# Optimization experiments

Measured on AMD Instinct MI355X. Metric: run time of the kernel, lower is better.

## Reference

```python
import jax, jax.numpy as jnp
import numpy as np

NU = 0.01 / np.pi  # Burgers viscosity
LAYERS = [2, 128, 128, 128, 128, 1]
N_EQ, N_INIT, N_BND = 131072, 4096, 4096


def setup_inputs() -> dict:
    key = jax.random.key(0)
    ks = jax.random.split(key, 16)
    inp = {
        'tx_equation': jax.random.uniform(ks[0], (N_EQ, 2), dtype=jnp.float32),
        'tx_init': jax.random.uniform(ks[1], (N_INIT, 2), dtype=jnp.float32),
        'tx_bound': jax.random.uniform(ks[2], (N_BND, 2), dtype=jnp.float32),
    }
    # Glorot-normal initialized Dense weights, zero biases (keras defaults in build_network)
    for i, (fin, fout) in enumerate(zip(LAYERS[:-1], LAYERS[1:])):
        std = np.sqrt(2.0 / (fin + fout)).astype(np.float32)
        inp[f'W{i}'] = jax.random.normal(ks[3 + i], (fin, fout), dtype=jnp.float32) * std
        inp[f'b{i}'] = jnp.zeros((fout,), dtype=jnp.float32)
    return inp


def _mlp_scalar(tx, Ws, bs):
    # tx: (2,) -> scalar u. tanh hidden layers, linear output.
    h = tx
    for W, b in zip(Ws[:-1], bs[:-1]):
        h = jnp.tanh(h @ W + b)
    return (h @ Ws[-1] + bs[-1])[0]


def reference(tx_equation, tx_init, tx_bound, W0, b0, W1, b1, W2, b2, W3, b3, W4, b4):
    Ws = [W0, W1, W2, W3, W4]
    bs = [b0, b1, b2, b3, b4]

    def u_s(tx):
        return _mlp_scalar(tx, Ws, bs)

    def u_x_s(tx):
        return jax.grad(u_s)(tx)[1]

    # PDE residual on collocation points
    u = jax.vmap(u_s)(tx_equation)                     # (N,)
    g = jax.vmap(jax.grad(u_s))(tx_equation)           # (N, 2) -> columns (u_t, u_x)
    u_t, u_x = g[:, 0], g[:, 1]
    u_xx = jax.vmap(jax.grad(u_x_s))(tx_equation)[:, 1]  # (N,)
    burgers_eq = (u_t + u * u_x - NU * u_xx)[:, None]     # (N, 1)

    # Initial / boundary predictions (single fused batch like tf.concat in call)
    tx_ib = jnp.concatenate([tx_init, tx_bound], axis=0)
    u_ib = jax.vmap(u_s)(tx_ib)[:, None]
    n_i = tx_init.shape[0]
    return burgers_eq, u_ib[:n_i], u_ib[n_i:]
```

## Files before the change

kernel.cpp:

```cpp
#include <hip/hip_runtime.h>
#include <math.h>

#define NU_F 0.0031830988618379067f
#define HS 136

typedef __attribute__((ext_vector_type(8))) _Float16 half8;
typedef __attribute__((ext_vector_type(4))) _Float16 half4;
typedef __attribute__((ext_vector_type(16))) float f32x16;

__device__ __forceinline__ float fast_tanh(float x) {
    const float e = __builtin_amdgcn_exp2f(x * 2.8853900817779268f);
    const float r = __builtin_amdgcn_rcpf(e + 1.f);
    return fmaf(-2.f, r, 1.f);
}

__global__ void prep_kernel(const float* __restrict__ W1,
                            const float* __restrict__ W2,
                            const float* __restrict__ W3,
                            _Float16* __restrict__ ws)
{
    const int g = blockIdx.x * 256 + threadIdx.x;
    const int l = g >> 14;
    const int r = g & 16383;
    const int n = r & 127;
    const int k = r >> 7;
    const float* W = (l == 0) ? W1 : (l == 1) ? W2 : W3;
    const float w = W[k * 128 + n];
    ws[l * 16384 + (k >> 4) * 2048 + n * 16 + (k & 15)] = (_Float16)w;
}

__launch_bounds__(256, 5)
__global__ void pinn_kernel(const float* __restrict__ tx_eq,
                            const float* __restrict__ tx_init,
                            const float* __restrict__ tx_bnd,
                            const float* __restrict__ W0, const float* __restrict__ b0,
                            const float* __restrict__ b1, const float* __restrict__ b2,
                            const float* __restrict__ b3,
                            const float* __restrict__ W4, const float* __restrict__ b4,
                            const _Float16* __restrict__ wt,
                            float* __restrict__ out)
{
    __shared__ _Float16 Hh[64][HS];

    const int tid   = threadIdx.x;
    const int blk   = blockIdx.x;
    const bool is_eq = (blk < 8192);
    const int w     = tid >> 6;
    const int lane  = tid & 63;
    const int col   = lane & 31;
    const int khalf = lane >> 5;
    const int ncol  = 32 * w + col;
    const int wofs  = ncol * 16 + khalf * 8;

    if (is_eq) {
        const int p  = tid >> 4;
        const int fb = (tid & 15) * 8;
        const float tv = tx_eq[blk * 32 + 2 * p];
        const float xv = tx_eq[blk * 32 + 2 * p + 1];
        const int m0 = 4 * p;
        float vch[4][8];
        #pragma unroll
        for (int j = 0; j < 8; ++j) {
            const int f = fb + j;
            const float w0v = W0[f];
            const float w1v = W0[128 + f];
            const float z = fmaf(tv, w0v, fmaf(xv, w1v, b0[f]));
            const float a = fast_tanh(z);
            const float s = 1.f - a * a;
            vch[0][j] = a;
            vch[1][j] = s * w0v;
            vch[2][j] = s * w1v;
            vch[3][j] = -2.f * a * s * w1v * w1v;
        }
        #pragma unroll
        for (int c = 0; c < 4; ++c) {
            half8 hh;
            #pragma unroll
            for (int j = 0; j < 8; ++j) hh[j] = (_Float16)vch[c][j];
            *(half8*)&Hh[m0 + c][fb] = hh;
        }
    } else {
        const int p  = tid >> 2;
        const int f0 = (tid & 3) * 32;
        const int gp = (blk - 8192) * 64 + p;
        const float* src = (gp < 4096) ? tx_init : tx_bnd;
        const int idx = (gp < 4096) ? gp : gp - 4096;
        const float tv = src[2 * idx];
        const float xv = src[2 * idx + 1];
        #pragma unroll
        for (int g = 0; g < 4; ++g) {
            half8 hh;
            #pragma unroll
            for (int j = 0; j < 8; ++j) {
                const int f = f0 + 8 * g + j;
                hh[j] = (_Float16)fast_tanh(fmaf(tv, W0[f], fmaf(xv, W0[128 + f], b0[f])));
            }
            *(half8*)&Hh[p][f0 + 8 * g] = hh;
        }
    }
    __syncthreads();

    const float* barr[3] = {b1, b2, b3};

    #pragma unroll 1
    for (int layer = 0; layer < 3; ++layer) {
        const _Float16* __restrict__ ph = wt + layer * 16384 + wofs;
        const float bias = barr[layer][ncol];

        half8 q0 = *(const half8*)(ph);
        half8 q1 = *(const half8*)(ph + 2048);
        half8 q2 = *(const half8*)(ph + 4096);
        half8 q3 = *(const half8*)(ph + 6144);
        half8 q4 = *(const half8*)(ph + 8192);
        half8 q5 = *(const half8*)(ph + 10240);
        half8 q6 = *(const half8*)(ph + 12288);
        half8 q7 = *(const half8*)(ph + 14336);

        f32x16 acc0, acc1;
        #pragma unroll
        for (int e = 0; e < 16; ++e) {
            const float v = (is_eq && (e & 3) != 0) ? 0.f : bias;
            acc0[e] = v; acc1[e] = v;
        }

#define KSTEP(KT, Q)                                                          \
        {                                                                     \
            const int k0 = KT * 16 + khalf * 8;                               \
            const half8 ah0 = *(const half8*)&Hh[col][k0];                    \
            const half8 ah1 = *(const half8*)&Hh[32 + col][k0];               \
            acc0 = __builtin_amdgcn_mfma_f32_32x32x16_f16(ah0, Q, acc0, 0, 0, 0); \
            acc1 = __builtin_amdgcn_mfma_f32_32x32x16_f16(ah1, Q, acc1, 0, 0, 0); \
        }
        KSTEP(0, q0) KSTEP(1, q1) KSTEP(2, q2) KSTEP(3, q3)
        KSTEP(4, q4) KSTEP(5, q5) KSTEP(6, q6) KSTEP(7, q7)
#undef KSTEP

        half4 h16[2][4];
        #pragma unroll
        for (int mt = 0; mt < 2; ++mt)
            #pragma unroll
            for (int g = 0; g < 4; ++g) {
                const float A0 = (mt == 0 ? acc0 : acc1)[4 * g + 0];
                const float A1 = (mt == 0 ? acc0 : acc1)[4 * g + 1];
                const float A2 = (mt == 0 ? acc0 : acc1)[4 * g + 2];
                const float A3 = (mt == 0 ? acc0 : acc1)[4 * g + 3];
                half4 hv;
                if (is_eq) {
                    const float t = fast_tanh(A0);
                    const float s = 1.f - t * t;
                    hv[0] = (_Float16)t;
                    hv[1] = (_Float16)(s * A1);
                    hv[2] = (_Float16)(s * A2);
                    hv[3] = (_Float16)fmaf(s, A3, -2.f * t * s * A2 * A2);
                } else {
                    hv[0] = (_Float16)fast_tanh(A0);
                    hv[1] = (_Float16)fast_tanh(A1);
                    hv[2] = (_Float16)fast_tanh(A2);
                    hv[3] = (_Float16)fast_tanh(A3);
                }
                h16[mt][g] = hv;
            }

        __syncthreads();

        #pragma unroll
        for (int mt = 0; mt < 2; ++mt)
            #pragma unroll
            for (int g = 0; g < 4; ++g) {
                const int mrow0 = mt * 32 + 8 * g + 4 * khalf;
                Hh[mrow0 + 0][ncol] = h16[mt][g][0];
                Hh[mrow0 + 1][ncol] = h16[mt][g][1];
                Hh[mrow0 + 2][ncol] = h16[mt][g][2];
                Hh[mrow0 + 3][ncol] = h16[mt][g][3];
            }
        __syncthreads();
    }

    {
        const float b4v = b4[0];
        const int m = tid >> 2;
        const int q = tid & 3;
        float dot = 0.f;
        #pragma unroll
        for (int g = 0; g < 4; ++g) {
            const int f = 32 * q + 8 * g;
            const half8 hh = *(const half8*)&Hh[m][f];
            const float4 wa = *(const float4*)&W4[f];
            const float4 wb = *(const float4*)&W4[f + 4];
            dot = fmaf((float)hh[0], wa.x, dot);
            dot = fmaf((float)hh[1], wa.y, dot);
            dot = fmaf((float)hh[2], wa.z, dot);
            dot = fmaf((float)hh[3], wa.w, dot);
            dot = fmaf((float)hh[4], wb.x, dot);
            dot = fmaf((float)hh[5], wb.y, dot);
            dot = fmaf((float)hh[6], wb.z, dot);
            dot = fmaf((float)hh[7], wb.w, dot);
        }
        dot += __shfl_xor(dot, 1);
        dot += __shfl_xor(dot, 2);

        if (is_eq) {
            const int j = lane >> 4;
            const int base = 16 * j;
            const float uu   = __shfl(dot, base + 0) + b4v;
            const float utv  = __shfl(dot, base + 4);
            const float uxv  = __shfl(dot, base + 8);
            const float uxxv = __shfl(dot, base + 12);
            if ((lane & 15) == 0)
                out[blk * 16 + 4 * w + j] = fmaf(uu, uxv, utv) - NU_F * uxxv;
        } else {
            if (q == 0)
                out[131072 + (blk - 8192) * 64 + m] = dot + b4v;
        }
    }
}

extern "C" void kernel_launch(void* const* d_in, const int* in_sizes, int n_in,
                              void* d_out, int out_size, void* d_ws, size_t ws_size,
                              hipStream_t stream)
{
    const float* tx_eq   = (const float*)d_in[0];
    const float* tx_init = (const float*)d_in[1];
    const float* tx_bnd  = (const float*)d_in[2];
    const float* W0 = (const float*)d_in[3];
    const float* b0 = (const float*)d_in[4];
    const float* W1 = (const float*)d_in[5];
    const float* b1 = (const float*)d_in[6];
    const float* W2 = (const float*)d_in[7];
    const float* b2 = (const float*)d_in[8];
    const float* W3 = (const float*)d_in[9];
    const float* b3 = (const float*)d_in[10];
    const float* W4 = (const float*)d_in[11];
    const float* b4 = (const float*)d_in[12];
    float* out = (float*)d_out;
    _Float16* wt = (_Float16*)d_ws;

    hipLaunchKernelGGL(prep_kernel, dim3(192), dim3(256), 0, stream, W1, W2, W3, wt);
    hipLaunchKernelGGL(pinn_kernel, dim3(8320), dim3(256), 0, stream,
                       tx_eq, tx_init, tx_bnd, W0, b0, b1, b2, b3, W4, b4,
                       (const _Float16*)wt, out);
}
```

Baseline: 171.1 us.

## Tile waves 2x2 over rows/cols and vectorize LDS writeback via DPP quad transpose

Reassigns the four waves from a 1x4 column split to a 2x2 grid, so each wave loads one A fragment per k-step and reuses it across two N tiles instead of loading two A fragments against one B. Activation writeback now packs fp16 pairs, transposes within lane quads using DPP and byte-permute, then stores 8-byte vectors instead of scalar 2-byte LDS stores. This halves LDS read traffic per MFMA and cuts LDS store count, at the price of doubling per-wave weight registers (16 half8 fragments). Launch bounds occupancy drops from 5 to 4 to make room.

```diff
diff --git a/kernel.cpp b/kernel.cpp
--- a/kernel.cpp
+++ b/kernel.cpp
@@ -5,13 +5,35 @@
 #define HS 136
 
 typedef __attribute__((ext_vector_type(8))) _Float16 half8;
-typedef __attribute__((ext_vector_type(4))) _Float16 half4;
 typedef __attribute__((ext_vector_type(16))) float f32x16;
 
 __device__ __forceinline__ float fast_tanh(float x) {
     const float e = __builtin_amdgcn_exp2f(x * 2.8853900817779268f);
     const float r = __builtin_amdgcn_rcpf(e + 1.f);
     return fmaf(-2.f, r, 1.f);
+}
+
+__device__ __forceinline__ uint32_t pack2(float x, float y) {
+    union { _Float16 h[2]; uint32_t u; } r;
+    r.h[0] = (_Float16)x; r.h[1] = (_Float16)y;
+    return r.u;
+}
+
+template<int CTRL>
+__device__ __forceinline__ uint32_t qperm(uint32_t v) {
+    return (uint32_t)__builtin_amdgcn_update_dpp(0, (int)v, CTRL, 0xF, 0xF, true);
+}
+
+__device__ __forceinline__ void quad_transpose(uint32_t &A, uint32_t &B,
+                                               uint32_t selM, bool qup) {
+    const uint32_t X = qperm<0xB1>(A);
+    const uint32_t Y = qperm<0xB1>(B);
+    const uint32_t u = __builtin_amdgcn_perm(A, X, selM);
+    const uint32_t v = __builtin_amdgcn_perm(B, Y, selM);
+    const uint32_t U2 = qperm<0x4E>(u);
+    const uint32_t V2 = qperm<0x4E>(v);
+    A = qup ? V2 : u;
+    B = qup ? v  : U2;
 }
 
 __global__ void prep_kernel(const float* __restrict__ W1,
@@ -29,7 +51,7 @@
     ws[l * 16384 + (k >> 4) * 2048 + n * 16 + (k & 15)] = (_Float16)w;
 }
 
-__launch_bounds__(256, 5)
+__launch_bounds__(256, 4)
 __global__ void pinn_kernel(const float* __restrict__ tx_eq,
                             const float* __restrict__ tx_init,
                             const float* __restrict__ tx_bnd,
@@ -49,8 +71,12 @@
     const int lane  = tid & 63;
     const int col   = lane & 31;
     const int khalf = lane >> 5;
-    const int ncol  = 32 * w + col;
-    const int wofs  = ncol * 16 + khalf * 8;
+    const int wr    = w >> 1;
+    const int wc    = w & 1;
+    const int ncol0 = 64 * wc + col;
+    const int arow  = 32 * wr + col;
+    const uint32_t selM = (lane & 1) ? 0x07060302u : 0x01000504u;
+    const bool qup = (lane & 2) != 0;
 
     if (is_eq) {
         const int p  = tid >> 4;
@@ -104,8 +130,9 @@
 
     #pragma unroll 1
     for (int layer = 0; layer < 3; ++layer) {
-        const _Float16* __restrict__ ph = wt + layer * 16384 + wofs;
-        const float bias = barr[layer][ncol];
+        const _Float16* __restrict__ ph = wt + layer * 16384 + ncol0 * 16 + khalf * 8;
+        const float bias0 = barr[layer][ncol0];
+        const float bias1 = barr[layer][ncol0 + 32];
 
         half8 q0 = *(const half8*)(ph);
         half8 q1 = *(const half8*)(ph + 2048);
@@ -115,64 +142,76 @@
         half8 q5 = *(const half8*)(ph + 10240);
         half8 q6 = *(const half8*)(ph + 12288);
         half8 q7 = *(const half8*)(ph + 14336);
+        half8 r0 = *(const half8*)(ph + 512);
+        half8 r1 = *(const half8*)(ph + 512 + 2048);
+        half8 r2 = *(const half8*)(ph + 512 + 4096);
+        half8 r3 = *(const half8*)(ph + 512 + 6144);
+        half8 r4 = *(const half8*)(ph + 512 + 8192);
+        half8 r5 = *(const half8*)(ph + 512 + 10240);
+        half8 r6 = *(const half8*)(ph + 512 + 12288);
+        half8 r7 = *(const half8*)(ph + 512 + 14336);
 
         f32x16 acc0, acc1;
         #pragma unroll
         for (int e = 0; e < 16; ++e) {
-            const float v = (is_eq && (e & 3) != 0) ? 0.f : bias;
-            acc0[e] = v; acc1[e] = v;
-        }
-
-#define KSTEP(KT, Q)                                                          \
+            acc0[e] = (is_eq && (e & 3) != 0) ? 0.f : bias0;
+            acc1[e] = (is_eq && (e & 3) != 0) ? 0.f : bias1;
+        }
+
+#define KSTEP(KT, Q, R)                                                       \
         {                                                                     \
-            const int k0 = KT * 16 + khalf * 8;                               \
-            const half8 ah0 = *(const half8*)&Hh[col][k0];                    \
-            const half8 ah1 = *(const half8*)&Hh[32 + col][k0];               \
-            acc0 = __builtin_amdgcn_mfma_f32_32x32x16_f16(ah0, Q, acc0, 0, 0, 0); \
-            acc1 = __builtin_amdgcn_mfma_f32_32x32x16_f16(ah1, Q, acc1, 0, 0, 0); \
-        }
-        KSTEP(0, q0) KSTEP(1, q1) KSTEP(2, q2) KSTEP(3, q3)
-        KSTEP(4, q4) KSTEP(5, q5) KSTEP(6, q6) KSTEP(7, q7)
+            const half8 a = *(const half8*)&Hh[arow][KT * 16 + khalf * 8];    \
+            acc0 = __builtin_amdgcn_mfma_f32_32x32x16_f16(a, Q, acc0, 0, 0, 0); \
+            acc1 = __builtin_amdgcn_mfma_f32_32x32x16_f16(a, R, acc1, 0, 0, 0); \
+        }
+        KSTEP(0, q0, r0) KSTEP(1, q1, r1) KSTEP(2, q2, r2) KSTEP(3, q3, r3)
+        KSTEP(4, q4, r4) KSTEP(5, q5, r5) KSTEP(6, q6, r6) KSTEP(7, q7, r7)
 #undef KSTEP
 
-        half4 h16[2][4];
-        #pragma unroll
-        for (int mt = 0; mt < 2; ++mt)
+        uint32_t tA[2][4], tB[2][4];
+        #pragma unroll
+        for (int nt = 0; nt < 2; ++nt)
             #pragma unroll
             for (int g = 0; g < 4; ++g) {
-                const float A0 = (mt == 0 ? acc0 : acc1)[4 * g + 0];
-                const float A1 = (mt == 0 ? acc0 : acc1)[4 * g + 1];
-                const float A2 = (mt == 0 ? acc0 : acc1)[4 * g + 2];
-                const float A3 = (mt == 0 ? acc0 : acc1)[4 * g + 3];
-                half4 hv;
+                const float A0 = (nt == 0 ? acc0 : acc1)[4 * g + 0];
+                const float A1 = (nt == 0 ? acc0 : acc1)[4 * g + 1];
+                const float A2 = (nt == 0 ? acc0 : acc1)[4 * g + 2];
+                const float A3 = (nt == 0 ? acc0 : acc1)[4 * g + 3];
+                float h0, h1, h2, h3;
                 if (is_eq) {
                     const float t = fast_tanh(A0);
                     const float s = 1.f - t * t;
-                    hv[0] = (_Float16)t;
-                    hv[1] = (_Float16)(s * A1);
-                    hv[2] = (_Float16)(s * A2);
-                    hv[3] = (_Float16)fmaf(s, A3, -2.f * t * s * A2 * A2);
+                    h0 = t;
+                    h1 = s * A1;
+                    h2 = s * A2;
+                    h3 = fmaf(s, A3, -2.f * t * s * A2 * A2);
                 } else {
-                    hv[0] = (_Float16)fast_tanh(A0);
-                    hv[1] = (_Float16)fast_tanh(A1);
-                    hv[2] = (_Float16)fast_tanh(A2);
-                    hv[3] = (_Float16)fast_tanh(A3);
+                    h0 = fast_tanh(A0);
+                    h1 = fast_tanh(A1);
+                    h2 = fast_tanh(A2);
+                    h3 = fast_tanh(A3);
                 }
-                h16[mt][g] = hv;
+                uint32_t pa = pack2(h0, h1);
+                uint32_t pb = pack2(h2, h3);
+                quad_transpose(pa, pb, selM, qup);
+                tA[nt][g] = pa;
+                tB[nt][g] = pb;
             }
 
         __syncthreads();
 
-        #pragma unroll
-        for (int mt = 0; mt < 2; ++mt)
-            #pragma unroll
-            for (int g = 0; g < 4; ++g) {
-                const int mrow0 = mt * 32 + 8 * g + 4 * khalf;
-                Hh[mrow0 + 0][ncol] = h16[mt][g][0];
-                Hh[mrow0 + 1][ncol] = h16[mt][g][1];
-                Hh[mrow0 + 2][ncol] = h16[mt][g][2];
-                Hh[mrow0 + 3][ncol] = h16[mt][g][3];
-            }
+        {
+            _Float16* vst = &Hh[32 * wr + 4 * khalf + (lane & 3)][64 * wc + (col & ~3)];
+            #pragma unroll
+            for (int nt = 0; nt < 2; ++nt)
+                #pragma unroll
+                for (int g = 0; g < 4; ++g) {
+                    uint2 val;
+                    val.x = tA[nt][g];
+                    val.y = tB[nt][g];
+                    *(uint2*)(vst + g * 8 * HS + nt * 32) = val;
+                }
+        }
         __syncthreads();
     }
 
```

After: 178.5 us. +4.3%, slower.
